# Kernel tuning notes

Measured on AMD Instinct MI355X. Metric: run time of the kernel, lower is better.

Reference implementation:

```python
import jax, jax.numpy as jnp
import numpy as np

B, H, W, C = 2, 96, 192, 768
NH, HD = 12, 64
W0, W1 = 8, 8          # window size
S0, S1 = 4, 4          # shift size
N = W0 * W1
NW = (H // W0) * (W // W1)
HID = 3072             # mlp_ratio 4 * dim
SCALE = HD ** -0.5


def _ln(x, g, b):
    m = x.mean(-1, keepdims=True)
    v = ((x - m) ** 2).mean(-1, keepdims=True)
    return (x - m) * jax.lax.rsqrt(v + 1e-5) * g + b


def _partition(x):  # (B,H,W,C) -> (B*NW, W0, W1, C)
    Bb = x.shape[0]
    x = x.reshape(Bb, H // W0, W0, W // W1, W1, -1).transpose(0, 1, 3, 2, 4, 5)
    return x.reshape(-1, W0, W1, x.shape[-1])


def _reverse(w):  # (B*NW, W0, W1, C) -> (B,H,W,C)
    Cc = w.shape[-1]
    x = w.reshape(B, H // W0, W // W1, W0, W1, Cc).transpose(0, 1, 3, 2, 4, 5)
    return x.reshape(B, H, W, Cc)


def _rope2(x):  # axial 2D RoPE on (nB, W0, W1, HD): first half rotates over h, second over w
    dh = HD // 2

    def cs(L, d):
        inv = 1.0 / (10000.0 ** (jnp.arange(0, d, 2, dtype=jnp.float32) / d))
        ang = jnp.arange(L, dtype=jnp.float32)[:, None] * inv
        return jnp.cos(ang), jnp.sin(ang)

    def rot(xa, cos, sin):
        x1, x2 = xa[..., 0::2], xa[..., 1::2]
        return jnp.stack([x1 * cos - x2 * sin, x1 * sin + x2 * cos], -1).reshape(xa.shape)

    ch, sh = cs(W0, dh)
    cw, sw = cs(W1, dh)
    xh = rot(x[..., :dh], ch[:, None, :], sh[:, None, :])
    xw = rot(x[..., dh:], cw[None, :, :], sw[None, :, :])
    return jnp.concatenate([xh, xw], -1)


def _make_mask():
    # faithful port of BasicLayer.create_mask (2D path)
    img = np.zeros((H, W), np.float32)
    cnt = 0
    for hs in (slice(0, -W0), slice(-W0, -S0), slice(-S0, None)):
        for wsl in (slice(0, -W1), slice(-W1, 0), slice(0, None)):
            img[hs, wsl] = cnt
            cnt += 1
    mw = img.reshape(H // W0, W0, W // W1, W1).transpose(0, 2, 1, 3).reshape(NW, N)
    am = mw[:, None, :] - mw[:, :, None]
    return jnp.asarray(np.where(am != 0, -100.0, 0.0).astype(np.float32))


def setup_inputs():
    key = jax.random.key(0)
    ks = jax.random.split(key, 6)
    s = lambda k, shape, fan: jax.random.normal(k, shape, jnp.float32) * (fan ** -0.5)
    return dict(
        x=jax.random.normal(ks[0], (B, H * W, C), jnp.float32),
        mask=_make_mask(),
        w_qkv=s(ks[1], (3 * C, C), C), b_qkv=jnp.zeros((3 * C,), jnp.float32),
        w_proj=s(ks[2], (C, C), C), b_proj=jnp.zeros((C,), jnp.float32),
        g1=jnp.ones((C,), jnp.float32), b1=jnp.zeros((C,), jnp.float32),
        g2=jnp.ones((C,), jnp.float32), b2=jnp.zeros((C,), jnp.float32),
        w_fc1=s(ks[3], (HID, C), C), b_fc1=jnp.zeros((HID,), jnp.float32),
        w_fc2=s(ks[4], (C, HID), HID), b_fc2=jnp.zeros((C,), jnp.float32),
    )


def reference(x, mask, w_qkv, b_qkv, w_proj, b_proj, g1, b1, g2, b2,
              w_fc1, b_fc1, w_fc2, b_fc2):
    shortcut = x
    xi = x.reshape(B, H, W, C)
    xi = jnp.roll(xi, (-S0, -S1), axis=(1, 2))
    xw = _partition(xi).reshape(-1, N, C)  # (B*NW, N, C)
    B_ = xw.shape[0]
    qkv = (xw @ w_qkv.T + b_qkv).reshape(B_, N, 3, NH, HD).transpose(2, 0, 3, 1, 4)
    q, k, v = qkv[0], qkv[1], qkv[2]  # (B_, NH, N, HD)
    q = _rope2(q.reshape(-1, W0, W1, HD)).reshape(B_, NH, N, HD)
    k = _rope2(k.reshape(-1, W0, W1, HD)).reshape(B_, NH, N, HD)
    attn = jnp.einsum('bhnd,bhmd->bhnm', q * SCALE, k)
    attn = attn.reshape(B, NW, NH, N, N) + mask[None, :, None]
    attn = jax.nn.softmax(attn.reshape(B_, NH, N, N), axis=-1)
    out = jnp.einsum('bhnm,bhmd->bnhd', attn, v).reshape(B_, N, C)
    out = out @ w_proj.T + b_proj
    xr = _reverse(out.reshape(-1, W0, W1, C))
    xr = jnp.roll(xr, (S0, S1), axis=(1, 2)).reshape(B, H * W, C)
    x1 = _ln(shortcut + xr, g1, b1)          # post-norm residual, as in source
    h = jax.nn.relu(x1 @ w_fc1.T + b_fc1) @ w_fc2.T + b_fc2
    return _ln(x1 + h, g2, b2)
```

## Files before the change

kernel.cpp:

```cpp
#include <hip/hip_runtime.h>
#include <math.h>
#include <stddef.h>

#define NTOK   36864
#define CDIM   768
#define HIDDIM 3072
#define QKVDIM 2304

typedef unsigned short u16;
typedef unsigned int   u32;
typedef __attribute__((ext_vector_type(8))) short short8;
typedef __attribute__((ext_vector_type(4))) short short4v;
typedef __attribute__((ext_vector_type(4))) float f32x4;

__device__ __forceinline__ float bf2f(u16 h) { return __uint_as_float(((u32)h) << 16); }
__device__ __forceinline__ u16 f2bf(float f) {
  u32 u = __float_as_uint(f);
  u32 r = u + 0x7fffu + ((u >> 16) & 1u);
  return (u16)(r >> 16);
}

__device__ __forceinline__ int win_row_to_src(int r) {
  int n = r & 63;
  int wflat = r >> 6;
  int b = wflat / 288;
  int wi = wflat - b * 288;
  int wh = wi / 24;
  int ww = wi - wh * 24;
  int i0 = n >> 3, i1 = n & 7;
  int hh = wh * 8 + i0 + 4; if (hh >= 96)  hh -= 96;
  int wp = ww * 8 + i1 + 4; if (wp >= 192) wp -= 192;
  return b * 18432 + hh * 192 + wp;
}

__device__ __forceinline__ void load_lds16(const u16* g, u16* l) {
  __builtin_amdgcn_global_load_lds((const __attribute__((address_space(1))) void*)g,
                                   (__attribute__((address_space(3))) void*)l, 16, 0, 0);
}

template<int OUTBF, int RELU, int RES>
__launch_bounds__(512, 4)
__global__ void gemm128(const u16* __restrict__ A, const u16* __restrict__ Wt,
                        const float* __restrict__ bias, const u16* __restrict__ res,
                        void* __restrict__ Cout, int M, int N, int K,
                        int gridx, int nwg)
{
  const int orig = blockIdx.x;
  const int xcd  = orig & 7;
  const int q    = nwg >> 3, r8 = nwg & 7;
  const int wgid = (xcd < r8 ? xcd * (q + 1) : r8 * (q + 1) + (xcd - r8) * q) + (orig >> 3);
  int bn, bm;
  if (((gridx | nwg) & 1) == 0) {
    const int halfn = nwg >> 1, hc = gridx >> 1;
    const int half  = (wgid >= halfn) ? 1 : 0;
    const int w2    = wgid - half * halfn;
    bn = (w2 % hc + half * hc) * 128;
    bm = (w2 / hc) * 128;
  } else {
    bn = (wgid % gridx) * 128;
    bm = (wgid / gridx) * 128;
  }

  __shared__ __align__(16) u16 lds[2][2][128 * 64];

  const int t    = threadIdx.x;
  const int wv   = t >> 6, lane = t & 63;
  const int wm   = wv >> 2, wn = wv & 3;
  const int lr   = lane & 15, lg = lane >> 4;
  const int sr   = t >> 3;
  const int ss   = t & 7;

  const u16* Abase = A  + (size_t)bm * K;
  const u16* Bbase = Wt + (size_t)bn * K;

  const int nt = K >> 6;

  auto stage = [&](int kt, int b) {
    const int k0 = kt << 6;
#pragma unroll
    for (int j = 0; j < 2; j++) {
      int row  = j * 64 + sr;
      int slot = ss ^ (row & 7);
      load_lds16(Abase + (size_t)row * K + k0 + slot * 8, &lds[b][0][j * 4096 + t * 8]);
    }
#pragma unroll
    for (int j = 0; j < 2; j++) {
      int row  = j * 64 + sr;
      int slot = ss ^ (row & 7);
      load_lds16(Bbase + (size_t)row * K + k0 + slot * 8, &lds[b][1][j * 4096 + t * 8]);
    }
  };

  f32x4 acc[4][2] = {};

  stage(0, 0);
  stage(1, 1);

  for (int tt = 0; tt < nt; tt++) {
    const int cur = tt & 1;
    if (tt + 1 < nt) asm volatile("s_waitcnt vmcnt(4)" ::: "memory");
    else             asm volatile("s_waitcnt vmcnt(0)" ::: "memory");
    __builtin_amdgcn_s_barrier();

    const u16* Ab = &lds[cur][0][0];
    const u16* Bb = &lds[cur][1][0];

    short8 bfr[2][2], afr[2][2];
#pragma unroll
    for (int nf = 0; nf < 2; nf++)
#pragma unroll
      for (int ks = 0; ks < 2; ks++) {
        int row = wn * 32 + nf * 16 + lr;
        bfr[nf][ks] = *(const short8*)(Bb + row * 64 + (((ks * 4 + lg) ^ (row & 7)) << 3));
      }
#pragma unroll
    for (int mf = 0; mf < 2; mf++)
#pragma unroll
      for (int ks = 0; ks < 2; ks++) {
        int row = wm * 64 + mf * 16 + lr;
        afr[mf][ks] = *(const short8*)(Ab + row * 64 + (((ks * 4 + lg) ^ (row & 7)) << 3));
      }
    asm volatile("s_waitcnt lgkmcnt(0)" ::: "memory");
    __builtin_amdgcn_sched_barrier(0);
    __builtin_amdgcn_s_setprio(1);
#pragma unroll
    for (int ks = 0; ks < 2; ks++)
#pragma unroll
      for (int mf = 0; mf < 2; mf++)
#pragma unroll
        for (int nf = 0; nf < 2; nf++)
          acc[mf][nf] = __builtin_amdgcn_mfma_f32_16x16x32_bf16(bfr[nf][ks], afr[mf][ks], acc[mf][nf], 0, 0, 0);
    __builtin_amdgcn_s_setprio(0);

    short8 afr2[2][2];
#pragma unroll
    for (int mf = 0; mf < 2; mf++)
#pragma unroll
      for (int ks = 0; ks < 2; ks++) {
        int row = wm * 64 + (mf + 2) * 16 + lr;
        afr2[mf][ks] = *(const short8*)(Ab + row * 64 + (((ks * 4 + lg) ^ (row & 7)) << 3));
      }
    asm volatile("s_waitcnt lgkmcnt(0)" ::: "memory");
    __builtin_amdgcn_sched_barrier(0);
    __builtin_amdgcn_s_barrier();

    if (tt + 2 < nt) stage(tt + 2, cur);

    __builtin_amdgcn_s_setprio(1);
#pragma unroll
    for (int ks = 0; ks < 2; ks++)
#pragma unroll
      for (int mf = 0; mf < 2; mf++)
#pragma unroll
        for (int nf = 0; nf < 2; nf++)
          acc[mf + 2][nf] = __builtin_amdgcn_mfma_f32_16x16x32_bf16(bfr[nf][ks], afr2[mf][ks], acc[mf + 2][nf], 0, 0, 0);
    __builtin_amdgcn_s_setprio(0);
  }

#pragma unroll
  for (int mf = 0; mf < 4; mf++) {
    size_t row = (size_t)(bm + wm * 64 + mf * 16 + lr);
#pragma unroll
    for (int nf = 0; nf < 2; nf++) {
      int col0 = bn + wn * 32 + nf * 16 + lg * 4;
      float4 b4 = *(const float4*)(bias + col0);
      float v0 = acc[mf][nf][0] + b4.x;
      float v1 = acc[mf][nf][1] + b4.y;
      float v2 = acc[mf][nf][2] + b4.z;
      float v3 = acc[mf][nf][3] + b4.w;
      if (RELU) {
        v0 = fmaxf(v0, 0.f); v1 = fmaxf(v1, 0.f);
        v2 = fmaxf(v2, 0.f); v3 = fmaxf(v3, 0.f);
      }
      if (RES) {
        short4v rv = *(const short4v*)(res + row * N + col0);
        v0 += bf2f((u16)rv[0]); v1 += bf2f((u16)rv[1]);
        v2 += bf2f((u16)rv[2]); v3 += bf2f((u16)rv[3]);
      }
      if (OUTBF) {
        short4v o;
        o[0] = (short)f2bf(v0); o[1] = (short)f2bf(v1);
        o[2] = (short)f2bf(v2); o[3] = (short)f2bf(v3);
        *(short4v*)((u16*)Cout + row * N + col0) = o;
      } else {
        f32x4 o = {v0, v1, v2, v3};
        *(f32x4*)((float*)Cout + row * N + col0) = o;
      }
    }
  }
}

__launch_bounds__(256)
__global__ void gather_x_bf16(const float* __restrict__ x, u16* __restrict__ xg)
{
  const int t = threadIdx.x, wv = t >> 6, lane = t & 63;
  const int r = blockIdx.x * 4 + wv;
  const float4* src = (const float4*)(x + (size_t)win_row_to_src(r) * CDIM);
  short4v* dst = (short4v*)(xg + (size_t)r * CDIM);
#pragma unroll
  for (int e = 0; e < 3; e++) {
    float4 f = src[e * 64 + lane];
    short4v o;
    o[0] = (short)f2bf(f.x); o[1] = (short)f2bf(f.y);
    o[2] = (short)f2bf(f.z); o[3] = (short)f2bf(f.w);
    dst[e * 64 + lane] = o;
  }
}

__launch_bounds__(256)
__global__ void conv4_bf16(const float* __restrict__ s0, const float* __restrict__ s1,
                           const float* __restrict__ s2, const float* __restrict__ s3,
                           u16* __restrict__ out)
{
  const int i = blockIdx.x * 256 + threadIdx.x;
  const int e = i * 4;
  const float* src; int off;
  if (e < 1769472)      { src = s0; off = 0; }
  else if (e < 2359296) { src = s1; off = 1769472; }
  else if (e < 4718592) { src = s2; off = 2359296; }
  else                  { src = s3; off = 4718592; }
  float4 f = *(const float4*)(src + (e - off));
  short4v o;
  o[0] = (short)f2bf(f.x); o[1] = (short)f2bf(f.y);
  o[2] = (short)f2bf(f.z); o[3] = (short)f2bf(f.w);
  *(short4v*)(out + e) = o;
}

__launch_bounds__(256)
__global__ void attn_mfma(const u16* __restrict__ qkv, const float* __restrict__ mask,
                          u16* __restrict__ out)
{
  __shared__ u16 vt[4][4096];
  __shared__ u16 pbuf[4][4096];
  __shared__ float ropetab[512];

  const int t = threadIdx.x;
  {
    int p = t >> 3, pos = t & 7;
    float inv = __expf(-(float)(p & 15) * 0.5756462732485115f);
    float sv, cv;
    sincosf((float)pos * inv, &sv, &cv);
    ropetab[t * 2]     = cv;
    ropetab[t * 2 + 1] = sv;
  }
  __syncthreads();

  const int wv = t >> 6, lane = t & 63;
  const int lr = lane & 15, lg = lane >> 4;
  const int gp   = blockIdx.x * 4 + wv;
  const int head = gp % 12;
  const int lw   = gp / 12;
  const int widx = lw % 288;
  const u16* base = qkv + (size_t)lw * 64 * QKVDIM + head * 64;

  {
    const u16* vrow = base + 1536 + (size_t)lane * QKVDIM;
    u16* vb = vt[wv];
#pragma unroll
    for (int s = 0; s < 8; s++) {
      short8 v = *(const short8*)(vrow + s * 8);
#pragma unroll
      for (int j = 0; j < 8; j++) {
        int d = s * 8 + j;
        vb[d * 64 + ((((lane >> 3) ^ (d & 7)) << 3) | (lane & 7))] = (u16)v[j];
      }
    }
  }

  short8 aq[4][2], ak[4][2];
#pragma unroll
  for (int f = 0; f < 4; f++) {
#pragma unroll
    for (int ks = 0; ks < 2; ks++) {
      int n = f * 16 + lr;
      short8 qv = *(const short8*)(base + (size_t)n * QKVDIM + ks * 32 + lg * 8);
      short8 kv = *(const short8*)(base + (size_t)n * QKVDIM + 768 + ks * 32 + lg * 8);
      short8 qo, ko;
#pragma unroll
      for (int jj = 0; jj < 4; jj++) {
        int p   = ks * 16 + lg * 4 + jj;
        int pos = (p < 16) ? (n >> 3) : (n & 7);
        float cv = ropetab[(p * 8 + pos) * 2];
        float sv = ropetab[(p * 8 + pos) * 2 + 1];
        float q1 = bf2f((u16)qv[2 * jj]), q2 = bf2f((u16)qv[2 * jj + 1]);
        float k1 = bf2f((u16)kv[2 * jj]), k2 = bf2f((u16)kv[2 * jj + 1]);
        qo[2 * jj]     = (short)f2bf((q1 * cv - q2 * sv) * 0.125f);
        qo[2 * jj + 1] = (short)f2bf((q1 * sv + q2 * cv) * 0.125f);
        ko[2 * jj]     = (short)f2bf(k1 * cv - k2 * sv);
        ko[2 * jj + 1] = (short)f2bf(k1 * sv + k2 * cv);
      }
      aq[f][ks] = qo; ak[f][ks] = ko;
    }
  }

  f32x4 sf[4][4] = {};
#pragma unroll
  for (int ks = 0; ks < 2; ks++)
#pragma unroll
    for (int fn = 0; fn < 4; fn++)
#pragma unroll
      for (int fm = 0; fm < 4; fm++)
        sf[fn][fm] = __builtin_amdgcn_mfma_f32_16x16x32_bf16(aq[fn][ks], ak[fm][ks], sf[fn][fm], 0, 0, 0);

  const float* mrow = mask + (size_t)widx * 4096;
#pragma unroll
  for (int fn = 0; fn < 4; fn++)
#pragma unroll
    for (int fm = 0; fm < 4; fm++)
#pragma unroll
      for (int j = 0; j < 4; j++)
        sf[fn][fm][j] += mrow[(fn * 16 + lg * 4 + j) * 64 + fm * 16 + lr];

#pragma unroll
  for (int fn = 0; fn < 4; fn++) {
#pragma unroll
    for (int j = 0; j < 4; j++) {
      float m0 = fmaxf(fmaxf(sf[fn][0][j], sf[fn][1][j]),
                       fmaxf(sf[fn][2][j], sf[fn][3][j]));
      m0 = fmaxf(m0, __shfl_xor(m0, 1));
      m0 = fmaxf(m0, __shfl_xor(m0, 2));
      m0 = fmaxf(m0, __shfl_xor(m0, 4));
      m0 = fmaxf(m0, __shfl_xor(m0, 8));
      float s0 = 0.f;
#pragma unroll
      for (int fm = 0; fm < 4; fm++) {
        float e = __expf(sf[fn][fm][j] - m0);
        sf[fn][fm][j] = e;
        s0 += e;
      }
      s0 += __shfl_xor(s0, 1);
      s0 += __shfl_xor(s0, 2);
      s0 += __shfl_xor(s0, 4);
      s0 += __shfl_xor(s0, 8);
      float r = 1.f / s0;
#pragma unroll
      for (int fm = 0; fm < 4; fm++) sf[fn][fm][j] *= r;
    }
  }

  u16* pb = pbuf[wv];
#pragma unroll
  for (int fn = 0; fn < 4; fn++)
#pragma unroll
    for (int fm = 0; fm < 4; fm++)
#pragma unroll
      for (int j = 0; j < 4; j++) {
        int n = fn * 16 + lg * 4 + j, m = fm * 16 + lr;
        pb[n * 64 + ((((m >> 3) ^ (n & 7)) << 3) | (m & 7))] = f2bf(sf[fn][fm][j]);
      }
  asm volatile("s_waitcnt lgkmcnt(0)" ::: "memory");
  __builtin_amdgcn_sched_barrier(0);

  short8 ap[4][2], bvf[4][2];
#pragma unroll
  for (int f = 0; f < 4; f++)
#pragma unroll
    for (int ks = 0; ks < 2; ks++) {
      int rn = f * 16 + lr;
      ap[f][ks]  = *(const short8*)(pb     + rn * 64 + (((ks * 4 + lg) ^ (rn & 7)) << 3));
      bvf[f][ks] = *(const short8*)(vt[wv] + rn * 64 + (((ks * 4 + lg) ^ (rn & 7)) << 3));
    }
  f32x4 o[4][4] = {};
#pragma unroll
  for (int ks = 0; ks < 2; ks++)
#pragma unroll
    for (int fn = 0; fn < 4; fn++)
#pragma unroll
      for (int fd = 0; fd < 4; fd++)
        o[fn][fd] = __builtin_amdgcn_mfma_f32_16x16x32_bf16(bvf[fd][ks], ap[fn][ks], o[fn][fd], 0, 0, 0);

  u16* ob = out + ((size_t)lw * 64) * CDIM + head * 64;
#pragma unroll
  for (int fn = 0; fn < 4; fn++) {
    size_t nrow = (size_t)(fn * 16 + lr) * CDIM;
#pragma unroll
    for (int fd = 0; fd < 4; fd++) {
      int d0 = fd * 16 + lg * 4;
      short4v ov;
      ov[0] = (short)f2bf(o[fn][fd][0]);
      ov[1] = (short)f2bf(o[fn][fd][1]);
      ov[2] = (short)f2bf(o[fn][fd][2]);
      ov[3] = (short)f2bf(o[fn][fd][3]);
      *(short4v*)(ob + nrow + d0) = ov;
    }
  }
}

__launch_bounds__(256)
__global__ void ln1_kernel(const u16* __restrict__ xg, const u16* __restrict__ add,
                           const float* __restrict__ g, const float* __restrict__ bb,
                           u16* __restrict__ out)
{
  const int t = threadIdx.x, wv = t >> 6, lane = t & 63;
  const int tok = blockIdx.x * 4 + wv;
  int b = tok / 18432;
  int hw = tok - b * 18432;
  int h = hw / 192, w = hw - h * 192;
  int h2 = h - 4; if (h2 < 0) h2 += 96;
  int w2 = w - 4; if (w2 < 0) w2 += 192;
  int r = ((b * 12 + (h2 >> 3)) * 24 + (w2 >> 3)) * 64 + (h2 & 7) * 8 + (w2 & 7);
  const short4v* a0 = (const short4v*)(xg  + (size_t)r * CDIM);
  const short4v* a1 = (const short4v*)(add + (size_t)r * CDIM);

  float v[12];
  float s1 = 0.f, s2 = 0.f;
#pragma unroll
  for (int e = 0; e < 3; e++) {
    short4v f = a0[e * 64 + lane];
    short4v a = a1[e * 64 + lane];
#pragma unroll
    for (int j = 0; j < 4; j++) {
      float x = bf2f((u16)f[j]) + bf2f((u16)a[j]);
      v[e*4+j] = x; s1 += x; s2 += x * x;
    }
  }
#pragma unroll
  for (int m = 1; m < 64; m <<= 1) {
    s1 += __shfl_xor(s1, m);
    s2 += __shfl_xor(s2, m);
  }
  float mean = s1 * (1.f / 768.f);
  float var  = s2 * (1.f / 768.f) - mean * mean;
  float rs   = rsqrtf(var + 1e-5f);
  short4v* dst = (short4v*)(out + (size_t)tok * CDIM);
#pragma unroll
  for (int e = 0; e < 3; e++) {
    short4v o;
#pragma unroll
    for (int j = 0; j < 4; j++) {
      int c = (e * 64 + lane) * 4 + j;
      o[j] = (short)f2bf((v[e*4+j] - mean) * rs * g[c] + bb[c]);
    }
    dst[e * 64 + lane] = o;
  }
}

__launch_bounds__(256)
__global__ void ln2_kernel(const u16* __restrict__ xin, const float* __restrict__ g,
                           const float* __restrict__ bb, float* __restrict__ out)
{
  const int t = threadIdx.x, wv = t >> 6, lane = t & 63;
  const int tok = blockIdx.x * 4 + wv;
  const short4v* a0 = (const short4v*)(xin + (size_t)tok * CDIM);

  float v[12];
  float s1 = 0.f, s2 = 0.f;
#pragma unroll
  for (int e = 0; e < 3; e++) {
    short4v a = a0[e * 64 + lane];
#pragma unroll
    for (int j = 0; j < 4; j++) {
      float x = bf2f((u16)a[j]);
      v[e*4+j] = x; s1 += x; s2 += x * x;
    }
  }
#pragma unroll
  for (int m = 1; m < 64; m <<= 1) {
    s1 += __shfl_xor(s1, m);
    s2 += __shfl_xor(s2, m);
  }
  float mean = s1 * (1.f / 768.f);
  float var  = s2 * (1.f / 768.f) - mean * mean;
  float rs   = rsqrtf(var + 1e-5f);
  float4* dst = (float4*)(out + (size_t)tok * CDIM);
#pragma unroll
  for (int e = 0; e < 3; e++) {
    float4 o;
    int c = (e * 64 + lane) * 4;
    o.x = (v[e*4+0] - mean) * rs * g[c+0] + bb[c+0];
    o.y = (v[e*4+1] - mean) * rs * g[c+1] + bb[c+1];
    o.z = (v[e*4+2] - mean) * rs * g[c+2] + bb[c+2];
    o.w = (v[e*4+3] - mean) * rs * g[c+3] + bb[c+3];
    dst[e * 64 + lane] = o;
  }
}

static inline void launch_gemm(const u16* A, const u16* Wt, const float* bias,
                               const u16* res, void* C, int M, int N, int K,
                               int outbf, int relu, int resf, hipStream_t s)
{
  int gridx = N / 128, nwg = gridx * (M / 128);
  if (outbf) {
    if (relu)      gemm128<1,1,0><<<nwg, 512, 0, s>>>(A, Wt, bias, res, C, M, N, K, gridx, nwg);
    else if (resf) gemm128<1,0,1><<<nwg, 512, 0, s>>>(A, Wt, bias, res, C, M, N, K, gridx, nwg);
    else           gemm128<1,0,0><<<nwg, 512, 0, s>>>(A, Wt, bias, res, C, M, N, K, gridx, nwg);
  } else {
    gemm128<0,0,0><<<nwg, 512, 0, s>>>(A, Wt, bias, res, C, M, N, K, gridx, nwg);
  }
}

extern "C" void kernel_launch(void* const* d_in, const int* in_sizes, int n_in,
                              void* d_out, int out_size, void* d_ws, size_t ws_size,
                              hipStream_t stream)
{
  const float* x      = (const float*)d_in[0];
  const float* mask   = (const float*)d_in[1];
  const float* w_qkv  = (const float*)d_in[2];
  const float* b_qkv  = (const float*)d_in[3];
  const float* w_proj = (const float*)d_in[4];
  const float* b_proj = (const float*)d_in[5];
  const float* g1     = (const float*)d_in[6];
  const float* b1     = (const float*)d_in[7];
  const float* g2     = (const float*)d_in[8];
  const float* b2     = (const float*)d_in[9];
  const float* w_fc1  = (const float*)d_in[10];
  const float* b_fc1  = (const float*)d_in[11];
  const float* w_fc2  = (const float*)d_in[12];
  const float* b_fc2  = (const float*)d_in[13];
  float* out = (float*)d_out;

  char* base = (char*)d_ws;
  u16* A0 = (u16*)base;
  u16* A1 = (u16*)(base + 56623104);
  u16* A2 = (u16*)(base + 226492416);
  u16* Hb = (u16*)base;
  u16* wqkvb  = (u16*)(base + 283115520);
  u16* wprojb = wqkvb  + 1769472;
  u16* wfc1b  = wprojb + 589824;
  u16* wfc2b  = wfc1b  + 2359296;

  conv4_bf16<<<1769472 / 256, 256, 0, stream>>>(w_qkv, w_proj, w_fc1, w_fc2, wqkvb);
  gather_x_bf16<<<NTOK / 4, 256, 0, stream>>>(x, A0);

  launch_gemm(A0, wqkvb, b_qkv, nullptr, A1, NTOK, QKVDIM, CDIM, 1, 0, 0, stream);
  attn_mfma<<<576 * 12 / 4, 256, 0, stream>>>(A1, mask, A2);

  launch_gemm(A2, wprojb, b_proj, nullptr, A1, NTOK, CDIM, CDIM, 1, 0, 0, stream);

  ln1_kernel<<<NTOK / 4, 256, 0, stream>>>(A0, A1, g1, b1, A2);

  launch_gemm(A2, wfc1b, b_fc1, nullptr, Hb, NTOK, HIDDIM, CDIM, 1, 1, 0, stream);
  launch_gemm(Hb, wfc2b, b_fc2, A2, A2, NTOK, CDIM, HIDDIM, 1, 0, 1, stream);

  ln2_kernel<<<NTOK / 4, 256, 0, stream>>>(A2, g2, b2, out);
}
```

Before: 854.8 us.

## Add 256x256-tile 8-phase pipelined GEMM for the MLP layers

Adds a new bf16 MFMA GEMM kernel with 256x256 output tiles and double-buffered LDS. Each K-tile is split into half-tile phases that interleave async global-to-LDS staging with MFMA blocks, separated by barriers and priority hints. The two MLP GEMMs (fc1 with ReLU, fc2 with residual) now use it, which raises data reuse per loaded tile and overlaps loads with compute. The cost is larger LDS use and registers per workgroup (launch bounds drop to 2 blocks), fewer workgroups in the grid, and many more barriers per iteration.

```diff
diff --git a/kernel.cpp b/kernel.cpp
--- a/kernel.cpp
+++ b/kernel.cpp
@@ -36,6 +36,175 @@
 __device__ __forceinline__ void load_lds16(const u16* g, u16* l) {
   __builtin_amdgcn_global_load_lds((const __attribute__((address_space(1))) void*)g,
                                    (__attribute__((address_space(3))) void*)l, 16, 0, 0);
+}
+
+#define GBAR()  __builtin_amdgcn_s_barrier()
+#define LGKM0() do { asm volatile("s_waitcnt lgkmcnt(0)" ::: "memory"); \
+                     __builtin_amdgcn_sched_barrier(0); } while (0)
+#define VMC4()  asm volatile("s_waitcnt vmcnt(4)" ::: "memory")
+
+template<int OUTBF, int RELU, int RES>
+__launch_bounds__(512, 2)
+__global__ void gemm256ph(const u16* __restrict__ A, const u16* __restrict__ Wt,
+                          const float* __restrict__ bias, const u16* __restrict__ res,
+                          void* __restrict__ Cout, int M, int N, int K,
+                          int gridx, int nwg)
+{
+  const int orig = blockIdx.x;
+  const int xcd  = orig & 7;
+  const int q    = nwg >> 3, r8 = nwg & 7;
+  const int wgid = (xcd < r8 ? xcd * (q + 1) : r8 * (q + 1) + (xcd - r8) * q) + (orig >> 3);
+  int bn, bm;
+  if (((gridx | nwg) & 1) == 0) {
+    const int halfn = nwg >> 1, hc = gridx >> 1;
+    const int half  = (wgid >= halfn) ? 1 : 0;
+    const int w2    = wgid - half * halfn;
+    bn = (w2 % hc + half * hc) * 256;
+    bm = (w2 / hc) * 256;
+  } else {
+    bn = (wgid % gridx) * 256;
+    bm = (wgid / gridx) * 256;
+  }
+
+  __shared__ __align__(16) u16 lds[2][2][256 * 64];
+
+  const int t    = threadIdx.x;
+  const int wv   = t >> 6, lane = t & 63;
+  const int wm   = wv >> 2, wn = wv & 3;
+  const int lr   = lane & 15, lg = lane >> 4;
+  const int sr   = t >> 3;
+  const int ss   = t & 7;
+
+  const u16* Abase = A  + (size_t)bm * K;
+  const u16* Bbase = Wt + (size_t)bn * K;
+
+  const int nt = K >> 6;
+
+  auto stageA = [&](int kt, int h, int b) {
+    const int k0 = kt << 6;
+#pragma unroll
+    for (int j = 0; j < 2; j++) {
+      int row  = j * 128 + h * 64 + sr;
+      int slot = ss ^ (row & 7);
+      load_lds16(Abase + (size_t)row * K + k0 + slot * 8, &lds[b][0][row * 64 + ss * 8]);
+    }
+  };
+  auto stageB = [&](int kt, int h, int b) {
+    const int k0 = kt << 6;
+#pragma unroll
+    for (int j = 0; j < 2; j++) {
+      int row  = (j * 2 + (sr >> 5)) * 64 + h * 32 + (sr & 31);
+      int slot = ss ^ (row & 7);
+      load_lds16(Bbase + (size_t)row * K + k0 + slot * 8, &lds[b][1][row * 64 + ss * 8]);
+    }
+  };
+
+  short8 afr[4][2], bfr0[2][2], bfr1[2][2];
+  auto lda = [&](const u16* Ab, int mh) {
+#pragma unroll
+    for (int mf = 0; mf < 4; mf++)
+#pragma unroll
+      for (int ks = 0; ks < 2; ks++) {
+        int row = wm * 128 + mh * 64 + mf * 16 + lr;
+        afr[mf][ks] = *(const short8*)(Ab + row * 64 + (((ks * 4 + lg) ^ (row & 7)) << 3));
+      }
+  };
+  auto ldb = [&](const u16* Bb, int nh, short8 bf[2][2]) {
+#pragma unroll
+    for (int nf = 0; nf < 2; nf++)
+#pragma unroll
+      for (int ks = 0; ks < 2; ks++) {
+        int row = wn * 64 + nh * 32 + nf * 16 + lr;
+        bf[nf][ks] = *(const short8*)(Bb + row * 64 + (((ks * 4 + lg) ^ (row & 7)) << 3));
+      }
+  };
+
+  f32x4 acc[8][4] = {};
+  auto mfma16 = [&](short8 bf[2][2], int mh, int nh) {
+    __builtin_amdgcn_s_setprio(1);
+#pragma unroll
+    for (int ks = 0; ks < 2; ks++)
+#pragma unroll
+      for (int mf = 0; mf < 4; mf++)
+#pragma unroll
+        for (int nf = 0; nf < 2; nf++)
+          acc[mh * 4 + mf][nh * 2 + nf] =
+            __builtin_amdgcn_mfma_f32_16x16x32_bf16(bf[nf][ks], afr[mf][ks],
+                                                    acc[mh * 4 + mf][nh * 2 + nf], 0, 0, 0);
+    __builtin_amdgcn_s_setprio(0);
+  };
+
+  const u16* A0 = &lds[0][0][0]; const u16* B0 = &lds[0][1][0];
+  const u16* A1 = &lds[1][0][0]; const u16* B1 = &lds[1][1][0];
+
+  stageA(0, 0, 0); stageB(0, 0, 0); stageA(0, 1, 0); stageB(0, 1, 0);
+  stageA(1, 0, 1); stageB(1, 0, 1);
+  VMC4();
+  GBAR();
+
+  const int nIter = nt >> 1;
+  for (int i = 0; i < nIter; i++) {
+    const int ka = 2 * i + 1, kb = 2 * i + 2, kc = 2 * i + 3;
+    const bool sb = kb < nt, sc = kc < nt;
+    lda(A0, 0); ldb(B0, 0, bfr0);
+    stageA(ka, 1, 1);
+    GBAR(); LGKM0(); mfma16(bfr0, 0, 0); GBAR();
+    ldb(B0, 1, bfr1);
+    stageB(ka, 1, 1);
+    GBAR(); LGKM0(); mfma16(bfr1, 0, 1); GBAR();
+    lda(A0, 1);
+    if (sb) stageA(kb, 0, 0);
+    GBAR(); LGKM0(); mfma16(bfr0, 1, 0); GBAR();
+    if (sb) stageB(kb, 0, 0);
+    GBAR(); LGKM0(); mfma16(bfr1, 1, 1);
+    VMC4();
+    GBAR();
+    lda(A1, 0); ldb(B1, 0, bfr0);
+    if (sb) stageA(kb, 1, 0);
+    GBAR(); LGKM0(); mfma16(bfr0, 0, 0); GBAR();
+    ldb(B1, 1, bfr1);
+    if (sb) stageB(kb, 1, 0);
+    GBAR(); LGKM0(); mfma16(bfr1, 0, 1); GBAR();
+    lda(A1, 1);
+    if (sc) stageA(kc, 0, 1);
+    GBAR(); LGKM0(); mfma16(bfr0, 1, 0); GBAR();
+    if (sc) stageB(kc, 0, 1);
+    GBAR(); LGKM0(); mfma16(bfr1, 1, 1);
+    VMC4();
+    GBAR();
+  }
+
+#pragma unroll
+  for (int mf = 0; mf < 8; mf++) {
+    size_t row = (size_t)(bm + wm * 128 + mf * 16 + lr);
+#pragma unroll
+    for (int nf = 0; nf < 4; nf++) {
+      int col0 = bn + wn * 64 + nf * 16 + lg * 4;
+      float4 b4 = *(const float4*)(bias + col0);
+      float v0 = acc[mf][nf][0] + b4.x;
+      float v1 = acc[mf][nf][1] + b4.y;
+      float v2 = acc[mf][nf][2] + b4.z;
+      float v3 = acc[mf][nf][3] + b4.w;
+      if (RELU) {
+        v0 = fmaxf(v0, 0.f); v1 = fmaxf(v1, 0.f);
+        v2 = fmaxf(v2, 0.f); v3 = fmaxf(v3, 0.f);
+      }
+      if (RES) {
+        short4v rv = *(const short4v*)(res + row * N + col0);
+        v0 += bf2f((u16)rv[0]); v1 += bf2f((u16)rv[1]);
+        v2 += bf2f((u16)rv[2]); v3 += bf2f((u16)rv[3]);
+      }
+      if (OUTBF) {
+        short4v o;
+        o[0] = (short)f2bf(v0); o[1] = (short)f2bf(v1);
+        o[2] = (short)f2bf(v2); o[3] = (short)f2bf(v3);
+        *(short4v*)((u16*)Cout + row * N + col0) = o;
+      } else {
+        f32x4 o = {v0, v1, v2, v3};
+        *(f32x4*)((float*)Cout + row * N + col0) = o;
+      }
+    }
+  }
 }
 
 template<int OUTBF, int RELU, int RES>
@@ -487,6 +656,16 @@
   } else {
     gemm128<0,0,0><<<nwg, 512, 0, s>>>(A, Wt, bias, res, C, M, N, K, gridx, nwg);
   }
+}
+
+static inline void launch_gemm8ph(const u16* A, const u16* Wt, const float* bias,
+                                  const u16* res, void* C, int M, int N, int K,
+                                  int relu, int resf, hipStream_t s)
+{
+  int gridx = N / 256, nwg = gridx * (M / 256);
+  if (relu)      gemm256ph<1,1,0><<<nwg, 512, 0, s>>>(A, Wt, bias, res, C, M, N, K, gridx, nwg);
+  else if (resf) gemm256ph<1,0,1><<<nwg, 512, 0, s>>>(A, Wt, bias, res, C, M, N, K, gridx, nwg);
+  else           gemm256ph<1,0,0><<<nwg, 512, 0, s>>>(A, Wt, bias, res, C, M, N, K, gridx, nwg);
 }
 
 extern "C" void kernel_launch(void* const* d_in, const int* in_sizes, int n_in,
@@ -529,8 +708,8 @@
 
   ln1_kernel<<<NTOK / 4, 256, 0, stream>>>(A0, A1, g1, b1, A2);
 
-  launch_gemm(A2, wfc1b, b_fc1, nullptr, Hb, NTOK, HIDDIM, CDIM, 1, 1, 0, stream);
-  launch_gemm(Hb, wfc2b, b_fc2, A2, A2, NTOK, CDIM, HIDDIM, 1, 0, 1, stream);
+  launch_gemm8ph(A2, wfc1b, b_fc1, nullptr, Hb, NTOK, HIDDIM, CDIM, 1, 0, stream);
+  launch_gemm8ph(Hb, wfc2b, b_fc2, A2, A2, NTOK, CDIM, HIDDIM, 0, 1, stream);
 
   ln2_kernel<<<NTOK / 4, 256, 0, stream>>>(A2, g2, b2, out);
 }
```

New measurement: 1.158 ms. 1.35x slower.

## Load GEMM B fragments directly to registers and deepen A LDS ring to four

Applied to the files above, without the earlier changes.

The GEMM kernel no longer stages the weight (B) tile through LDS. Each wave loads its B fragments straight from global memory into registers, prefetched one k-step ahead. The activation (A) tile now uses a four-deep LDS ring filled three steps ahead, which removes the second barrier and the split MFMA phase in each iteration. The cost is redundant global B reads across waves that share the same wn, and unswizzled, latency-exposed register loads. The vmcnt(4) wait also counts the newly issued B loads, so it may drain the A prefetches early and reduce the effective pipeline depth.

```diff
diff --git a/kernel.cpp b/kernel.cpp
--- a/kernel.cpp
+++ b/kernel.cpp
@@ -38,12 +38,14 @@
                                    (__attribute__((address_space(3))) void*)l, 16, 0, 0);
 }
 
+#define SB() __builtin_amdgcn_sched_barrier(0)
+
 template<int OUTBF, int RELU, int RES>
 __launch_bounds__(512, 4)
-__global__ void gemm128(const u16* __restrict__ A, const u16* __restrict__ Wt,
-                        const float* __restrict__ bias, const u16* __restrict__ res,
-                        void* __restrict__ Cout, int M, int N, int K,
-                        int gridx, int nwg)
+__global__ void gemm128b(const u16* __restrict__ A, const u16* __restrict__ Wt,
+                         const float* __restrict__ bias, const u16* __restrict__ res,
+                         void* __restrict__ Cout, int M, int N, int K,
+                         int gridx, int nwg)
 {
   const int orig = blockIdx.x;
   const int xcd  = orig & 7;
@@ -61,7 +63,7 @@
     bm = (wgid / gridx) * 128;
   }
 
-  __shared__ __align__(16) u16 lds[2][2][128 * 64];
+  __shared__ __align__(16) u16 ldsA[4][128 * 64];
 
   const int t    = threadIdx.x;
   const int wv   = t >> 6, lane = t & 63;
@@ -75,46 +77,52 @@
 
   const int nt = K >> 6;
 
-  auto stage = [&](int kt, int b) {
+  auto stageA = [&](int kt, int b) {
     const int k0 = kt << 6;
 #pragma unroll
     for (int j = 0; j < 2; j++) {
       int row  = j * 64 + sr;
       int slot = ss ^ (row & 7);
-      load_lds16(Abase + (size_t)row * K + k0 + slot * 8, &lds[b][0][j * 4096 + t * 8]);
-    }
-#pragma unroll
-    for (int j = 0; j < 2; j++) {
-      int row  = j * 64 + sr;
-      int slot = ss ^ (row & 7);
-      load_lds16(Bbase + (size_t)row * K + k0 + slot * 8, &lds[b][1][j * 4096 + t * 8]);
+      load_lds16(Abase + (size_t)row * K + k0 + slot * 8, &ldsA[b][j * 4096 + t * 8]);
     }
   };
-
-  f32x4 acc[4][2] = {};
-
-  stage(0, 0);
-  stage(1, 1);
-
-  for (int tt = 0; tt < nt; tt++) {
-    const int cur = tt & 1;
-    if (tt + 1 < nt) asm volatile("s_waitcnt vmcnt(4)" ::: "memory");
-    else             asm volatile("s_waitcnt vmcnt(0)" ::: "memory");
-    __builtin_amdgcn_s_barrier();
-
-    const u16* Ab = &lds[cur][0][0];
-    const u16* Bb = &lds[cur][1][0];
-
-    short8 bfr[2][2], afr[2][2];
+  auto loadB = [&](int kt, short8 bf[2][2]) {
+    const int k0 = kt << 6;
 #pragma unroll
     for (int nf = 0; nf < 2; nf++)
 #pragma unroll
       for (int ks = 0; ks < 2; ks++) {
         int row = wn * 32 + nf * 16 + lr;
-        bfr[nf][ks] = *(const short8*)(Bb + row * 64 + (((ks * 4 + lg) ^ (row & 7)) << 3));
-      }
-#pragma unroll
-    for (int mf = 0; mf < 2; mf++)
+        bf[nf][ks] = *(const short8*)(Bbase + (size_t)row * K + k0 + ks * 32 + lg * 8);
+      }
+  };
+
+  f32x4 acc[4][2] = {};
+  short8 bcur[2][2], bnxt[2][2];
+
+  stageA(0, 0); stageA(1, 1); stageA(2, 2);
+  loadB(0, bnxt);
+
+  for (int tt = 0; tt < nt; tt++) {
+#pragma unroll
+    for (int nf = 0; nf < 2; nf++)
+#pragma unroll
+      for (int ks = 0; ks < 2; ks++)
+        bcur[nf][ks] = bnxt[nf][ks];
+    SB();
+    if (tt + 1 < nt) loadB(tt + 1, bnxt);
+    SB();
+    if (tt < nt - 3) asm volatile("s_waitcnt vmcnt(4)" ::: "memory");
+    else             asm volatile("s_waitcnt vmcnt(0)" ::: "memory");
+    SB();
+    __builtin_amdgcn_s_barrier();
+    SB();
+    if (tt + 3 < nt) stageA(tt + 3, (tt + 3) & 3);
+    SB();
+    const u16* Ab = &ldsA[tt & 3][0];
+    short8 afr[4][2];
+#pragma unroll
+    for (int mf = 0; mf < 4; mf++)
 #pragma unroll
       for (int ks = 0; ks < 2; ks++) {
         int row = wm * 64 + mf * 16 + lr;
@@ -126,34 +134,10 @@
 #pragma unroll
     for (int ks = 0; ks < 2; ks++)
 #pragma unroll
-      for (int mf = 0; mf < 2; mf++)
+      for (int mf = 0; mf < 4; mf++)
 #pragma unroll
         for (int nf = 0; nf < 2; nf++)
-          acc[mf][nf] = __builtin_amdgcn_mfma_f32_16x16x32_bf16(bfr[nf][ks], afr[mf][ks], acc[mf][nf], 0, 0, 0);
-    __builtin_amdgcn_s_setprio(0);
-
-    short8 afr2[2][2];
-#pragma unroll
-    for (int mf = 0; mf < 2; mf++)
-#pragma unroll
-      for (int ks = 0; ks < 2; ks++) {
-        int row = wm * 64 + (mf + 2) * 16 + lr;
-        afr2[mf][ks] = *(const short8*)(Ab + row * 64 + (((ks * 4 + lg) ^ (row & 7)) << 3));
-      }
-    asm volatile("s_waitcnt lgkmcnt(0)" ::: "memory");
-    __builtin_amdgcn_sched_barrier(0);
-    __builtin_amdgcn_s_barrier();
-
-    if (tt + 2 < nt) stage(tt + 2, cur);
-
-    __builtin_amdgcn_s_setprio(1);
-#pragma unroll
-    for (int ks = 0; ks < 2; ks++)
-#pragma unroll
-      for (int mf = 0; mf < 2; mf++)
-#pragma unroll
-        for (int nf = 0; nf < 2; nf++)
-          acc[mf + 2][nf] = __builtin_amdgcn_mfma_f32_16x16x32_bf16(bfr[nf][ks], afr2[mf][ks], acc[mf + 2][nf], 0, 0, 0);
+          acc[mf][nf] = __builtin_amdgcn_mfma_f32_16x16x32_bf16(bcur[nf][ks], afr[mf][ks], acc[mf][nf], 0, 0, 0);
     __builtin_amdgcn_s_setprio(0);
   }
 
@@ -481,11 +465,11 @@
 {
   int gridx = N / 128, nwg = gridx * (M / 128);
   if (outbf) {
-    if (relu)      gemm128<1,1,0><<<nwg, 512, 0, s>>>(A, Wt, bias, res, C, M, N, K, gridx, nwg);
-    else if (resf) gemm128<1,0,1><<<nwg, 512, 0, s>>>(A, Wt, bias, res, C, M, N, K, gridx, nwg);
-    else           gemm128<1,0,0><<<nwg, 512, 0, s>>>(A, Wt, bias, res, C, M, N, K, gridx, nwg);
+    if (relu)      gemm128b<1,1,0><<<nwg, 512, 0, s>>>(A, Wt, bias, res, C, M, N, K, gridx, nwg);
+    else if (resf) gemm128b<1,0,1><<<nwg, 512, 0, s>>>(A, Wt, bias, res, C, M, N, K, gridx, nwg);
+    else           gemm128b<1,0,0><<<nwg, 512, 0, s>>>(A, Wt, bias, res, C, M, N, K, gridx, nwg);
   } else {
-    gemm128<0,0,0><<<nwg, 512, 0, s>>>(A, Wt, bias, res, C, M, N, K, gridx, nwg);
+    gemm128b<0,0,0><<<nwg, 512, 0, s>>>(A, Wt, bias, res, C, M, N, K, gridx, nwg);
   }
 }
 
```

New measurement: 1.378 ms. 61.2% more time.

## Add 32x32x16 MFMA GEMM variant with XCD remap for MLP layers

Applied to the files above, without the earlier changes.

Adds a new 128x128-tile GEMM kernel that uses 32x32x16 bf16 MFMA instructions with two accumulators per wave. It double-buffers swizzled LDS tiles, interleaves LDS fragment loads with MFMA issue under s_setprio, and remaps workgroups across XCDs so neighbouring tiles share L2. Only the two MLP GEMMs (fc1 and fc2) use it. The intent is higher matrix-core throughput and better cache locality on the largest GEMMs, at the cost of more register pressure and a hand-tuned wait/barrier schedule that could be fragile.

```diff
diff --git a/kernel.cpp b/kernel.cpp
--- a/kernel.cpp
+++ b/kernel.cpp
@@ -12,6 +12,7 @@
 typedef __attribute__((ext_vector_type(8))) short short8;
 typedef __attribute__((ext_vector_type(4))) short short4v;
 typedef __attribute__((ext_vector_type(4))) float f32x4;
+typedef __attribute__((ext_vector_type(16))) float f32x16;
 
 __device__ __forceinline__ float bf2f(u16 h) { return __uint_as_float(((u32)h) << 16); }
 __device__ __forceinline__ u16 f2bf(float f) {
@@ -190,6 +191,147 @@
   }
 }
 
+template<int OUTBF, int RELU, int RES>
+__launch_bounds__(512, 4)
+__global__ void gemm128w(const u16* __restrict__ A, const u16* __restrict__ Wt,
+                         const float* __restrict__ bias, const u16* __restrict__ res,
+                         void* __restrict__ Cout, int M, int N, int K,
+                         int gridx, int nwg)
+{
+  const int orig = blockIdx.x;
+  const int xcd  = orig & 7;
+  const int q    = nwg >> 3, r8 = nwg & 7;
+  const int wgid = (xcd < r8 ? xcd * (q + 1) : r8 * (q + 1) + (xcd - r8) * q) + (orig >> 3);
+  int bn, bm;
+  if (((gridx | nwg) & 1) == 0) {
+    const int halfn = nwg >> 1, hc = gridx >> 1;
+    const int half  = (wgid >= halfn) ? 1 : 0;
+    const int w2    = wgid - half * halfn;
+    bn = (w2 % hc + half * hc) * 128;
+    bm = (w2 / hc) * 128;
+  } else {
+    bn = (wgid % gridx) * 128;
+    bm = (wgid / gridx) * 128;
+  }
+
+  __shared__ __align__(16) u16 lds[2][2][128 * 64];
+
+  const int t    = threadIdx.x;
+  const int wv   = t >> 6, lane = t & 63;
+  const int wm   = wv >> 2, wn = wv & 3;
+  const int l31  = lane & 31, hi = lane >> 5;
+  const int sr   = t >> 3;
+  const int ss   = t & 7;
+
+  const u16* Abase = A  + (size_t)bm * K;
+  const u16* Bbase = Wt + (size_t)bn * K;
+
+  const int nt = K >> 6;
+
+  auto stage = [&](int kt, int b) {
+    const int k0 = kt << 6;
+#pragma unroll
+    for (int j = 0; j < 2; j++) {
+      int row  = j * 64 + sr;
+      int slot = ss ^ (row & 7);
+      load_lds16(Abase + (size_t)row * K + k0 + slot * 8, &lds[b][0][j * 4096 + t * 8]);
+    }
+#pragma unroll
+    for (int j = 0; j < 2; j++) {
+      int row  = j * 64 + sr;
+      int slot = ss ^ (row & 7);
+      load_lds16(Bbase + (size_t)row * K + k0 + slot * 8, &lds[b][1][j * 4096 + t * 8]);
+    }
+  };
+
+  f32x16 acc0 = {};
+  f32x16 acc1 = {};
+
+  stage(0, 0);
+  stage(1, 1);
+
+  const int rowb = wn * 32 + l31;
+  const int rowa0 = wm * 64 + l31;
+  const int rowa1 = wm * 64 + 32 + l31;
+
+  for (int tt = 0; tt < nt; tt++) {
+    const int cur = tt & 1;
+    if (tt + 1 < nt) asm volatile("s_waitcnt vmcnt(4)" ::: "memory");
+    else             asm volatile("s_waitcnt vmcnt(0)" ::: "memory");
+    __builtin_amdgcn_s_barrier();
+
+    const u16* Ab = &lds[cur][0][0];
+    const u16* Bb = &lds[cur][1][0];
+
+    short8 bfr[4], afr[4];
+#pragma unroll
+    for (int ks = 0; ks < 4; ks++)
+      bfr[ks] = *(const short8*)(Bb + rowb * 64 + (((ks * 2 + hi) ^ (rowb & 7)) << 3));
+#pragma unroll
+    for (int ks = 0; ks < 4; ks++)
+      afr[ks] = *(const short8*)(Ab + rowa0 * 64 + (((ks * 2 + hi) ^ (rowa0 & 7)) << 3));
+    asm volatile("s_waitcnt lgkmcnt(0)" ::: "memory");
+    __builtin_amdgcn_sched_barrier(0);
+    __builtin_amdgcn_s_setprio(1);
+#pragma unroll
+    for (int ks = 0; ks < 4; ks++)
+      acc0 = __builtin_amdgcn_mfma_f32_32x32x16_bf16(bfr[ks], afr[ks], acc0, 0, 0, 0);
+    __builtin_amdgcn_s_setprio(0);
+
+    short8 afr2[4];
+#pragma unroll
+    for (int ks = 0; ks < 4; ks++)
+      afr2[ks] = *(const short8*)(Ab + rowa1 * 64 + (((ks * 2 + hi) ^ (rowa1 & 7)) << 3));
+    asm volatile("s_waitcnt lgkmcnt(0)" ::: "memory");
+    __builtin_amdgcn_sched_barrier(0);
+    __builtin_amdgcn_s_barrier();
+
+    if (tt + 2 < nt) stage(tt + 2, cur);
+
+    __builtin_amdgcn_s_setprio(1);
+#pragma unroll
+    for (int ks = 0; ks < 4; ks++)
+      acc1 = __builtin_amdgcn_mfma_f32_32x32x16_bf16(bfr[ks], afr2[ks], acc1, 0, 0, 0);
+    __builtin_amdgcn_s_setprio(0);
+  }
+
+#pragma unroll
+  for (int mf = 0; mf < 2; mf++) {
+    size_t row = (size_t)(bm + wm * 64 + mf * 32 + l31);
+#pragma unroll
+    for (int g = 0; g < 4; g++) {
+      int col0 = bn + wn * 32 + g * 8 + hi * 4;
+      float4 b4 = *(const float4*)(bias + col0);
+      float a0 = mf ? acc1[g * 4 + 0] : acc0[g * 4 + 0];
+      float a1 = mf ? acc1[g * 4 + 1] : acc0[g * 4 + 1];
+      float a2 = mf ? acc1[g * 4 + 2] : acc0[g * 4 + 2];
+      float a3 = mf ? acc1[g * 4 + 3] : acc0[g * 4 + 3];
+      float v0 = a0 + b4.x;
+      float v1 = a1 + b4.y;
+      float v2 = a2 + b4.z;
+      float v3 = a3 + b4.w;
+      if (RELU) {
+        v0 = fmaxf(v0, 0.f); v1 = fmaxf(v1, 0.f);
+        v2 = fmaxf(v2, 0.f); v3 = fmaxf(v3, 0.f);
+      }
+      if (RES) {
+        short4v rv = *(const short4v*)(res + row * N + col0);
+        v0 += bf2f((u16)rv[0]); v1 += bf2f((u16)rv[1]);
+        v2 += bf2f((u16)rv[2]); v3 += bf2f((u16)rv[3]);
+      }
+      if (OUTBF) {
+        short4v o;
+        o[0] = (short)f2bf(v0); o[1] = (short)f2bf(v1);
+        o[2] = (short)f2bf(v2); o[3] = (short)f2bf(v3);
+        *(short4v*)((u16*)Cout + row * N + col0) = o;
+      } else {
+        f32x4 o = {v0, v1, v2, v3};
+        *(f32x4*)((float*)Cout + row * N + col0) = o;
+      }
+    }
+  }
+}
+
 __launch_bounds__(256)
 __global__ void gather_x_bf16(const float* __restrict__ x, u16* __restrict__ xg)
 {
@@ -487,6 +629,16 @@
   } else {
     gemm128<0,0,0><<<nwg, 512, 0, s>>>(A, Wt, bias, res, C, M, N, K, gridx, nwg);
   }
+}
+
+static inline void launch_gemm_w(const u16* A, const u16* Wt, const float* bias,
+                                 const u16* res, void* C, int M, int N, int K,
+                                 int relu, int resf, hipStream_t s)
+{
+  int gridx = N / 128, nwg = gridx * (M / 128);
+  if (relu)      gemm128w<1,1,0><<<nwg, 512, 0, s>>>(A, Wt, bias, res, C, M, N, K, gridx, nwg);
+  else if (resf) gemm128w<1,0,1><<<nwg, 512, 0, s>>>(A, Wt, bias, res, C, M, N, K, gridx, nwg);
+  else           gemm128w<1,0,0><<<nwg, 512, 0, s>>>(A, Wt, bias, res, C, M, N, K, gridx, nwg);
 }
 
 extern "C" void kernel_launch(void* const* d_in, const int* in_sizes, int n_in,
@@ -529,8 +681,8 @@
 
   ln1_kernel<<<NTOK / 4, 256, 0, stream>>>(A0, A1, g1, b1, A2);
 
-  launch_gemm(A2, wfc1b, b_fc1, nullptr, Hb, NTOK, HIDDIM, CDIM, 1, 1, 0, stream);
-  launch_gemm(Hb, wfc2b, b_fc2, A2, A2, NTOK, CDIM, HIDDIM, 1, 0, 1, stream);
+  launch_gemm_w(A2, wfc1b, b_fc1, nullptr, Hb, NTOK, HIDDIM, CDIM, 1, 0, stream);
+  launch_gemm_w(Hb, wfc2b, b_fc2, A2, A2, NTOK, CDIM, HIDDIM, 0, 1, stream);
 
   ln2_kernel<<<NTOK / 4, 256, 0, stream>>>(A2, g2, b2, out);
 }
```

After: 915.6 us. 1.07x slower.
